# Optimization experiments

Measured on AMD Instinct MI355X. Metric: run time of the kernel, lower is better.

Reference implementation:

```python
import jax, jax.numpy as jnp
import numpy as np

B, N, MODEL_D = 2, 1024, 2048
KQ_D, V_D, H, I = 128, 128, 8, 4
ROPE_THETA = 10000.0


def _rope(x, theta):
    # x: [b, n, ..., d]; positions along axis 1, rotation over last dim d.
    d = x.shape[-1]
    n = x.shape[1]
    inv_freq = theta ** (-jnp.arange(0, d, 2, dtype=jnp.float32) / d)  # [d/2]
    ang = jnp.arange(n, dtype=jnp.float32)[:, None] * inv_freq          # [n, d/2]
    bshape = (1, n) + (1,) * (x.ndim - 3) + (d // 2,)
    cos = jnp.cos(ang).reshape(bshape).astype(x.dtype)
    sin = jnp.sin(ang).reshape(bshape).astype(x.dtype)
    x1, x2 = jnp.split(x, 2, axis=-1)
    return jnp.concatenate([x1 * cos - x2 * sin, x1 * sin + x2 * cos], axis=-1)


def setup_inputs() -> dict:
    key = jax.random.key(0)
    kx, kq, kk, kv, ko = jax.random.split(key, 5)
    s_in = 1.0 / np.sqrt(MODEL_D)
    s_out = 1.0 / np.sqrt(H * I * V_D)
    x = jax.random.normal(kx, (B, N, MODEL_D), jnp.float32)
    Wq = jax.random.normal(kq, (MODEL_D, H, I, KQ_D), jnp.float32) * s_in
    Wk = jax.random.normal(kk, (MODEL_D, H, KQ_D), jnp.float32) * s_in
    Wv = jax.random.normal(kv, (MODEL_D, H, V_D), jnp.float32) * s_in
    Wo = jax.random.normal(ko, (H, I, V_D, MODEL_D), jnp.float32) * s_out
    return {"x": x, "Wq": Wq, "Wk": Wk, "Wv": Wv, "Wo": Wo}


def reference(x, Wq, Wk, Wv, Wo):
    # GQA projections (per Ueajsum specs)
    q = jnp.einsum('bnd,dhik->bnhik', x, Wq)   # [B,N,H,I,K]
    k = jnp.einsum('bnd,dhc->bnhc', x, Wk)     # [B,N,H,K]
    v = jnp.einsum('bnd,dhv->bnhv', x, Wv)     # [B,N,H,V]
    # RoPE on q and k
    q = _rope(q, ROPE_THETA)
    k = _rope(k, ROPE_THETA)
    # Causal softmax attention, each kv head serves I query heads
    scale = 1.0 / np.sqrt(KQ_D)
    scores = jnp.einsum('bnhic,bmhc->bhinm', q, k) * scale  # [B,H,I,N,N]
    n = x.shape[1]
    causal = jnp.tril(jnp.ones((n, n), dtype=bool))
    scores = jnp.where(causal, scores, jnp.finfo(scores.dtype).min)
    p = jax.nn.softmax(scores, axis=-1)
    out = jnp.einsum('bhinm,bmhv->bnhiv', p, v)              # [B,N,H,I,V]
    return jnp.einsum('bnhiv,hivd->bnd', out, Wo)            # [B,N,D]
```

## Files before the change

kernel.cpp:

```cpp
#include <hip/hip_runtime.h>
#include <hip/hip_bf16.h>

typedef __bf16 bf16x8 __attribute__((ext_vector_type(8)));
typedef float floatx4 __attribute__((ext_vector_type(4)));

static __device__ __forceinline__ void async_cp16(const __bf16* g, __bf16* l) {
    typedef const __attribute__((address_space(1))) unsigned int gu32;
    typedef __attribute__((address_space(3))) unsigned int lu32;
    __builtin_amdgcn_global_load_lds((gu32*)g, (lu32*)l, 16, 0, 0);
}

static __device__ __forceinline__ void tile64_f32(
    const float* __restrict__ src, __bf16* __restrict__ dst,
    int R, int C, int r0, int c0, int tid, __bf16* t )
{
    {
        const int r = tid >> 2, cq = (tid & 3) * 16;
        const float* p = src + (size_t)(r0 + r) * C + c0 + cq;
        float4 f0 = *(const float4*)(p);
        float4 f1 = *(const float4*)(p + 4);
        float4 f2 = *(const float4*)(p + 8);
        float4 f3 = *(const float4*)(p + 12);
        __bf16 v[16] = {
            (__bf16)f0.x, (__bf16)f0.y, (__bf16)f0.z, (__bf16)f0.w,
            (__bf16)f1.x, (__bf16)f1.y, (__bf16)f1.z, (__bf16)f1.w,
            (__bf16)f2.x, (__bf16)f2.y, (__bf16)f2.z, (__bf16)f2.w,
            (__bf16)f3.x, (__bf16)f3.y, (__bf16)f3.z, (__bf16)f3.w };
        #pragma unroll
        for (int e = 0; e < 16; ++e) t[(cq + e) * 72 + r] = v[e];
    }
    __syncthreads();
    {
        const int c = tid >> 2, rq = (tid & 3) * 16;
        uint4 u0 = *(const uint4*)(&t[c * 72 + rq]);
        uint4 u1 = *(const uint4*)(&t[c * 72 + rq + 8]);
        __bf16* q = dst + (size_t)(c0 + c) * R + r0 + rq;
        *(uint4*)(q)     = u0;
        *(uint4*)(q + 8) = u1;
    }
}

static __device__ __forceinline__ void tile64_b16(
    const __bf16* __restrict__ src, __bf16* __restrict__ dst,
    int src_ld, int dst_ld, int tid, __bf16* t )
{
    {
        const int r = tid >> 2, cq = (tid & 3) * 16;
        const __bf16* p = src + (size_t)r * src_ld + cq;
        union { uint4 u; __bf16 b[8]; } a0, a1;
        a0.u = *(const uint4*)(p);
        a1.u = *(const uint4*)(p + 8);
        #pragma unroll
        for (int e = 0; e < 8; ++e) {
            t[(cq + e) * 72 + r]     = a0.b[e];
            t[(cq + 8 + e) * 72 + r] = a1.b[e];
        }
    }
    __syncthreads();
    {
        const int c = tid >> 2, rq = (tid & 3) * 16;
        uint4 u0 = *(const uint4*)(&t[c * 72 + rq]);
        uint4 u1 = *(const uint4*)(&t[c * 72 + rq + 8]);
        __bf16* q = dst + (size_t)c * dst_ld + rq;
        *(uint4*)(q)     = u0;
        *(uint4*)(q + 8) = u1;
    }
}

__global__ __launch_bounds__(256) void prep_kernel(
    const float* __restrict__ x,  __bf16* __restrict__ xb,
    const float* __restrict__ Wq, const float* __restrict__ Wk,
    const float* __restrict__ Wv, __bf16* __restrict__ Wt)
{
    __shared__ __bf16 t[64 * 72];
    const int bk  = blockIdx.x;
    const int tid = threadIdx.x;

    if (bk < 2048) {
        int ct = bk & 63, rt = bk >> 6;
        tile64_f32(Wq, Wt, 2048, 4096, rt * 64, ct * 64, tid, t);
    } else if (bk < 2560) {
        int idx = bk - 2048, ct = idx & 15, rt = idx >> 4;
        tile64_f32(Wk, Wt + (size_t)4096 * 2048, 2048, 1024, rt * 64, ct * 64, tid, t);
    } else if (bk < 3072) {
        int idx = bk - 2560, ct = idx & 15, rt = idx >> 4;
        tile64_f32(Wv, Wt + (size_t)5120 * 2048, 2048, 1024, rt * 64, ct * 64, tid, t);
    } else {
        int idx = (bk - 3072) * 256 + tid;
        const float* p = x + (size_t)idx * 8;
        float4 f0 = *(const float4*)p;
        float4 f1 = *(const float4*)(p + 4);
        union { uint4 u; __bf16 b[8]; } o;
        o.b[0] = (__bf16)f0.x; o.b[1] = (__bf16)f0.y; o.b[2] = (__bf16)f0.z; o.b[3] = (__bf16)f0.w;
        o.b[4] = (__bf16)f1.x; o.b[5] = (__bf16)f1.y; o.b[6] = (__bf16)f1.z; o.b[7] = (__bf16)f1.w;
        *(uint4*)(xb + (size_t)idx * 8) = o.u;
    }
}

__global__ __launch_bounds__(256) void rope_vtrans_wot_kernel(
    __bf16* __restrict__ qkv, __bf16* __restrict__ vt,
    const float* __restrict__ Wo, __bf16* __restrict__ WoT)
{
    __shared__ __bf16 t[64 * 72];
    const int bk  = blockIdx.x;
    const int tid = threadIdx.x;

    if (bk < 2560) {
        int idx  = bk * 256 + tid;
        int part = idx & 7;
        int tt   = idx >> 3;
        int head = tt % 40;
        int row  = tt / 40;
        int n    = row & 1023;
        int col0 = (head < 32) ? head * 128 : 4096 + (head - 32) * 128;
        size_t base = (size_t)row * 6144 + col0 + part * 8;

        union { uint4 u; __bf16 b[8]; } x1, x2, o1, o2;
        x1.u = *(const uint4*)(qkv + base);
        x2.u = *(const uint4*)(qkv + base + 64);
        #pragma unroll
        for (int e = 0; e < 8; ++e) {
            int j = part * 8 + e;
            float inv_freq = exp2f(-(float)j * 0.20762050593046015f);
            float ang = (float)n * inv_freq;
            float sv, cv;
            __sincosf(ang, &sv, &cv);
            float a = (float)x1.b[e], b2 = (float)x2.b[e];
            o1.b[e] = (__bf16)(a * cv - b2 * sv);
            o2.b[e] = (__bf16)(a * sv + b2 * cv);
        }
        *(uint4*)(qkv + base)      = o1.u;
        *(uint4*)(qkv + base + 64) = o2.u;
    } else if (bk < 3072) {
        int idx = bk - 2560;
        int bh = idx >> 5, rem = idx & 31;
        int k0 = (rem >> 1) * 64, v0 = (rem & 1) * 64;
        int b = bh >> 3, h = bh & 7;
        const __bf16* src = qkv + (size_t)(b * 1024 + k0) * 6144 + 5120 + h * 128 + v0;
        __bf16* dst = vt + ((size_t)bh * 128 + v0) * 1024 + k0;
        tile64_b16(src, dst, 6144, 1024, tid, t);
    } else {
        int idx = bk - 3072;
        int ct = idx & 31, rt = idx >> 5;
        tile64_f32(Wo, WoT, 4096, 2048, rt * 64, ct * 64, tid, t);
    }
}

__global__ __launch_bounds__(512) void gemm_bt(
    const __bf16* __restrict__ A,
    const __bf16* __restrict__ Bt,
    __bf16* __restrict__ C,
    int M, int lda, int ldb, int ldc,
    int kc_base, int kc_extra)
{
    __shared__ __bf16 As[2][256 * 64];
    __shared__ __bf16 Bs[2][256 * 64];

    const int tid  = threadIdx.x;
    const int wave = tid >> 6;
    const int lane = tid & 63;
    const int quad = lane >> 4;
    const int l15  = lane & 15;
    const int wr   = wave >> 2;
    const int wc   = wave & 3;

    const int bm = blockIdx.y * 256;
    const int bn = blockIdx.x * 256;
    const int z  = blockIdx.z;
    const int Kc = kc_base + ((z == (int)gridDim.z - 1) ? kc_extra : 0);
    const int NT = Kc >> 6;

    A  += (size_t)z * kc_base;
    Bt += (size_t)z * kc_base;
    C  += (size_t)z * M * ldc;

    floatx4 acc[32];
    #pragma unroll
    for (int i = 0; i < 32; ++i) acc[i] = floatx4{0.f, 0.f, 0.f, 0.f};

    const int sr = lane >> 3;
    const int sc = ((lane & 7) ^ sr) * 8;
    const __bf16* a0 = A  + (size_t)(bm + wave * 8 + sr) * lda + sc;
    const __bf16* b0 = Bt + (size_t)(bn + wave * 8 + sr) * ldb + sc;
    const int ldsw = wave * 512;

    const int arow = (wr * 128 + l15) * 64;
    const int brow = (wc * 64  + l15) * 64;
    const int cx0  = ((0 + quad) ^ (l15 & 7)) * 8;
    const int cx1  = ((4 + quad) ^ (l15 & 7)) * 8;

    #pragma unroll
    for (int q = 0; q < 4; ++q)
        async_cp16(a0 + (size_t)(q * 64) * lda, (__bf16*)&As[0][q * 4096 + ldsw]);
    #pragma unroll
    for (int q = 0; q < 4; ++q)
        async_cp16(b0 + (size_t)(q * 64) * ldb, (__bf16*)&Bs[0][q * 4096 + ldsw]);
    if (NT > 1) {
        #pragma unroll
        for (int q = 0; q < 4; ++q)
            async_cp16(a0 + (size_t)(q * 64) * lda + 64, (__bf16*)&As[1][q * 4096 + ldsw]);
        #pragma unroll
        for (int q = 0; q < 4; ++q)
            async_cp16(b0 + (size_t)(q * 64) * ldb + 64, (__bf16*)&Bs[1][q * 4096 + ldsw]);
        asm volatile("s_waitcnt vmcnt(8)" ::: "memory");
    } else {
        asm volatile("s_waitcnt vmcnt(0)" ::: "memory");
    }
    __builtin_amdgcn_s_barrier();
    __builtin_amdgcn_sched_barrier(0);

    for (int t = 0; t < NT; ++t) {
        const int cur = t & 1;
        const __bf16* Ac = As[cur];
        const __bf16* Bc = Bs[cur];
        __bf16* An = (__bf16*)As[cur];
        __bf16* Bn = (__bf16*)Bs[cur];

        bf16x8 af[4][2], bfA[2][2], bfB[2][2];

        #pragma unroll
        for (int tt = 0; tt < 4; ++tt) {
            af[tt][0] = *(const bf16x8*)(&Ac[arow + tt * 1024 + cx0]);
            af[tt][1] = *(const bf16x8*)(&Ac[arow + tt * 1024 + cx1]);
        }
        #pragma unroll
        for (int uu = 0; uu < 2; ++uu) {
            bfA[uu][0] = *(const bf16x8*)(&Bc[brow + uu * 1024 + cx0]);
            bfA[uu][1] = *(const bf16x8*)(&Bc[brow + uu * 1024 + cx1]);
        }
        __builtin_amdgcn_s_barrier();
        asm volatile("s_waitcnt lgkmcnt(0)" ::: "memory");
        __builtin_amdgcn_sched_barrier(0);
        __builtin_amdgcn_s_setprio(1);
        #pragma unroll
        for (int ko = 0; ko < 2; ++ko)
            #pragma unroll
            for (int tt = 0; tt < 4; ++tt)
                #pragma unroll
                for (int uu = 0; uu < 2; ++uu)
                    acc[tt * 4 + uu] = __builtin_amdgcn_mfma_f32_16x16x32_bf16(
                        af[tt][ko], bfA[uu][ko], acc[tt * 4 + uu], 0, 0, 0);
        __builtin_amdgcn_s_setprio(0);
        __builtin_amdgcn_s_barrier();
        __builtin_amdgcn_sched_barrier(0);

        #pragma unroll
        for (int uu = 0; uu < 2; ++uu) {
            bfB[uu][0] = *(const bf16x8*)(&Bc[brow + (2 + uu) * 1024 + cx0]);
            bfB[uu][1] = *(const bf16x8*)(&Bc[brow + (2 + uu) * 1024 + cx1]);
        }
        __builtin_amdgcn_s_barrier();
        asm volatile("s_waitcnt lgkmcnt(0)" ::: "memory");
        __builtin_amdgcn_sched_barrier(0);
        __builtin_amdgcn_s_setprio(1);
        #pragma unroll
        for (int ko = 0; ko < 2; ++ko)
            #pragma unroll
            for (int tt = 0; tt < 4; ++tt)
                #pragma unroll
                for (int uu = 0; uu < 2; ++uu)
                    acc[tt * 4 + 2 + uu] = __builtin_amdgcn_mfma_f32_16x16x32_bf16(
                        af[tt][ko], bfB[uu][ko], acc[tt * 4 + 2 + uu], 0, 0, 0);
        __builtin_amdgcn_s_setprio(0);
        __builtin_amdgcn_s_barrier();
        __builtin_amdgcn_sched_barrier(0);

        #pragma unroll
        for (int tt = 0; tt < 4; ++tt) {
            af[tt][0] = *(const bf16x8*)(&Ac[arow + (4 + tt) * 1024 + cx0]);
            af[tt][1] = *(const bf16x8*)(&Ac[arow + (4 + tt) * 1024 + cx1]);
        }
        if (t + 2 < NT) {
            #pragma unroll
            for (int q = 0; q < 4; ++q)
                async_cp16(b0 + (size_t)(q * 64) * ldb + (t + 2) * 64,
                           Bn + q * 4096 + ldsw);
        }
        __builtin_amdgcn_s_barrier();
        asm volatile("s_waitcnt lgkmcnt(0)" ::: "memory");
        __builtin_amdgcn_sched_barrier(0);
        __builtin_amdgcn_s_setprio(1);
        #pragma unroll
        for (int ko = 0; ko < 2; ++ko)
            #pragma unroll
            for (int tt = 0; tt < 4; ++tt)
                #pragma unroll
                for (int uu = 0; uu < 2; ++uu)
                    acc[(4 + tt) * 4 + uu] = __builtin_amdgcn_mfma_f32_16x16x32_bf16(
                        af[tt][ko], bfA[uu][ko], acc[(4 + tt) * 4 + uu], 0, 0, 0);
        __builtin_amdgcn_s_setprio(0);
        __builtin_amdgcn_s_barrier();
        __builtin_amdgcn_sched_barrier(0);

        if (t + 2 < NT) {
            #pragma unroll
            for (int q = 0; q < 4; ++q)
                async_cp16(a0 + (size_t)(q * 64) * lda + (t + 2) * 64,
                           An + q * 4096 + ldsw);
        }
        __builtin_amdgcn_s_setprio(1);
        #pragma unroll
        for (int ko = 0; ko < 2; ++ko)
            #pragma unroll
            for (int tt = 0; tt < 4; ++tt)
                #pragma unroll
                for (int uu = 0; uu < 2; ++uu)
                    acc[(4 + tt) * 4 + 2 + uu] = __builtin_amdgcn_mfma_f32_16x16x32_bf16(
                        af[tt][ko], bfB[uu][ko], acc[(4 + tt) * 4 + 2 + uu], 0, 0, 0);
        __builtin_amdgcn_s_setprio(0);
        if (t + 2 < NT) {
            asm volatile("s_waitcnt vmcnt(8)" ::: "memory");
        } else {
            asm volatile("s_waitcnt vmcnt(0)" ::: "memory");
        }
        __builtin_amdgcn_s_barrier();
        __builtin_amdgcn_sched_barrier(0);
    }

    #pragma unroll
    for (int tt = 0; tt < 8; ++tt)
        #pragma unroll
        for (int uu = 0; uu < 4; ++uu) {
            const int row = bm + wr * 128 + tt * 16 + quad * 4;
            const int col = bn + wc * 64 + uu * 16 + l15;
            #pragma unroll
            for (int r = 0; r < 4; ++r)
                C[(size_t)(row + r) * ldc + col] = (__bf16)acc[tt * 4 + uu][r];
        }
}

__global__ __launch_bounds__(256) void reduce_kernel(
    const __bf16* __restrict__ part, float* __restrict__ out)
{
    int idx = blockIdx.x * 256 + threadIdx.x;
    const size_t S = (size_t)2048 * 2048;
    union { uint4 u; __bf16 b[8]; } p0, p1, p2;
    p0.u = *(const uint4*)(part + (size_t)idx * 8);
    p1.u = *(const uint4*)(part + S + (size_t)idx * 8);
    p2.u = *(const uint4*)(part + 2 * S + (size_t)idx * 8);
    float4 o0, o1;
    o0.x = (float)p0.b[0] + (float)p1.b[0] + (float)p2.b[0];
    o0.y = (float)p0.b[1] + (float)p1.b[1] + (float)p2.b[1];
    o0.z = (float)p0.b[2] + (float)p1.b[2] + (float)p2.b[2];
    o0.w = (float)p0.b[3] + (float)p1.b[3] + (float)p2.b[3];
    o1.x = (float)p0.b[4] + (float)p1.b[4] + (float)p2.b[4];
    o1.y = (float)p0.b[5] + (float)p1.b[5] + (float)p2.b[5];
    o1.z = (float)p0.b[6] + (float)p1.b[6] + (float)p2.b[6];
    o1.w = (float)p0.b[7] + (float)p1.b[7] + (float)p2.b[7];
    *(float4*)(out + (size_t)idx * 8)     = o0;
    *(float4*)(out + (size_t)idx * 8 + 4) = o1;
}

__global__ __launch_bounds__(512, 2) void attn_kernel(
    const __bf16* __restrict__ qkv,
    const __bf16* __restrict__ vt,
    __bf16* __restrict__ ao)
{
    const int PS_LD = 72;
    __shared__ __bf16 Ks[64 * 128];
    __shared__ __bf16 Vs[128 * 64];
    __shared__ __bf16 Ps[8][16 * PS_LD];

    const int tid  = threadIdx.x;
    const int wave = tid >> 6;
    const int lane = tid & 63;
    const int quad = lane >> 4;
    const int l15  = lane & 15;
    const int i    = wave >> 1;
    const int rt   = wave & 1;

    const int pair = blockIdx.x;
    const int bh   = blockIdx.y;
    const int b    = bh >> 3, h = bh & 7;
    const __bf16* vtb = vt + (size_t)bh * 128 * 1024;

    const int keyA = wave * 8 + (lane >> 4);
    const int keyB = keyA + 4;
    const int chA  = (lane & 15) ^ (keyA & 15);
    const int chB  = (lane & 15) ^ (keyB & 15);
    const __bf16* gK0 = qkv + (size_t)(b * 1024 + keyA) * 6144 + 4096 + h * 128 + chA * 8;
    const __bf16* gK1 = qkv + (size_t)(b * 1024 + keyB) * 6144 + 4096 + h * 128 + chB * 8;
    __bf16* lK0 = Ks + (wave * 8) * 128;
    __bf16* lK1 = Ks + (wave * 8 + 4) * 128;

    const int vdA = wave * 16 + (lane >> 3);
    const int vdB = vdA + 8;
    const int cvA = (lane & 7) ^ (vdA & 7);
    const int cvB = (lane & 7) ^ (vdB & 7);
    const __bf16* gV0 = vtb + (size_t)vdA * 1024 + cvA * 8;
    const __bf16* gV1 = vtb + (size_t)vdB * 1024 + cvB * 8;
    __bf16* lV0 = Vs + (wave * 16) * 64;
    __bf16* lV1 = Vs + (wave * 16 + 8) * 64;

    bf16x8 onesf;
    #pragma unroll
    for (int j = 0; j < 8; ++j) onesf[j] = (__bf16)1.0f;

    const float C2 = 0.12751898549f;

    #pragma unroll
    for (int ph = 0; ph < 2; ++ph) {
        const int qt    = ph ? (31 - pair) : pair;
        const int qrow0 = qt * 32 + rt * 16;

        const __bf16* qp = qkv + (size_t)(b * 1024 + qrow0 + l15) * 6144 + (h * 4 + i) * 128;
        bf16x8 qf[4];
        #pragma unroll
        for (int c = 0; c < 4; ++c)
            qf[c] = *(const bf16x8*)(qp + c * 32 + quad * 8);

        floatx4 acc[8];
        #pragma unroll
        for (int u = 0; u < 8; ++u) acc[u] = floatx4{0.f, 0.f, 0.f, 0.f};
        floatx4 accl = floatx4{0.f, 0.f, 0.f, 0.f};

        const int ntiles = (qt >> 1) + 1;
        for (int t = 0; t < ntiles; ++t) {
            const int kt = t * 64;
            __syncthreads();
            async_cp16(gK0 + (size_t)kt * 6144, lK0);
            async_cp16(gK1 + (size_t)kt * 6144, lK1);
            async_cp16(gV0 + kt, lV0);
            async_cp16(gV1 + kt, lV1);
            __syncthreads();

            floatx4 s[4];
            #pragma unroll
            for (int ks = 0; ks < 4; ++ks) s[ks] = floatx4{0.f, 0.f, 0.f, 0.f};
            #pragma unroll
            for (int c = 0; c < 4; ++c) {
                #pragma unroll
                for (int ks = 0; ks < 4; ++ks) {
                    bf16x8 kf = *(const bf16x8*)(
                        &Ks[(ks * 16 + l15) * 128 + ((c * 4 + quad) ^ l15) * 8]);
                    s[ks] = __builtin_amdgcn_mfma_f32_16x16x32_bf16(qf[c], kf, s[ks], 0, 0, 0);
                }
            }

            #pragma unroll
            for (int r = 0; r < 4; ++r) {
                int qrow = qrow0 + quad * 4 + r;
                #pragma unroll
                for (int ks = 0; ks < 4; ++ks) {
                    int kc = kt + ks * 16 + l15;
                    float p = (kc <= qrow) ? exp2f(s[ks][r] * C2) : 0.0f;
                    Ps[wave][(quad * 4 + r) * PS_LD + ks * 16 + l15] = (__bf16)p;
                }
            }

            #pragma unroll
            for (int s2 = 0; s2 < 2; ++s2) {
                bf16x8 pa = *(const bf16x8*)(&Ps[wave][l15 * PS_LD + s2 * 32 + quad * 8]);
                accl = __builtin_amdgcn_mfma_f32_16x16x32_bf16(pa, onesf, accl, 0, 0, 0);
                #pragma unroll
                for (int u = 0; u < 8; ++u) {
                    bf16x8 vf = *(const bf16x8*)(
                        &Vs[(u * 16 + l15) * 64 + (((s2 * 4 + quad) ^ (l15 & 7))) * 8]);
                    acc[u] = __builtin_amdgcn_mfma_f32_16x16x32_bf16(pa, vf, acc[u], 0, 0, 0);
                }
            }
        }

        #pragma unroll
        for (int r = 0; r < 4; ++r) {
            float inv = 1.0f / accl[r];
            int row = qrow0 + quad * 4 + r;
            __bf16* op = ao + (size_t)(b * 1024 + row) * 4096 + (h * 4 + i) * 128;
            #pragma unroll
            for (int u = 0; u < 8; ++u)
                op[u * 16 + l15] = (__bf16)(acc[u][r] * inv);
        }
    }
}

extern "C" void kernel_launch(void* const* d_in, const int* in_sizes, int n_in,
                              void* d_out, int out_size, void* d_ws, size_t ws_size,
                              hipStream_t stream)
{
    const float* x  = (const float*)d_in[0];
    const float* Wq = (const float*)d_in[1];
    const float* Wk = (const float*)d_in[2];
    const float* Wv = (const float*)d_in[3];
    const float* Wo = (const float*)d_in[4];
    float* out = (float*)d_out;

    const size_t MB = 1024 * 1024;
    char* ws = (char*)d_ws;
    __bf16* qkv  = (__bf16*)(ws);
    __bf16* vtb  = (__bf16*)(ws + 24 * MB);
    __bf16* xb   = (__bf16*)(ws + 28 * MB);
    __bf16* Wt   = (__bf16*)(ws + 36 * MB);
    __bf16* WoT  = (__bf16*)(ws + 28 * MB);
    __bf16* ao   = (__bf16*)(ws + 44 * MB);
    __bf16* part = (__bf16*)(ws);

    prep_kernel<<<5120, 256, 0, stream>>>(x, xb, Wq, Wk, Wv, Wt);
    gemm_bt<<<dim3(24, 8), 512, 0, stream>>>(xb, Wt, qkv, 2048, 2048, 2048, 6144, 2048, 0);
    rope_vtrans_wot_kernel<<<5120, 256, 0, stream>>>(qkv, vtb, Wo, WoT);
    attn_kernel<<<dim3(16, 16), 512, 0, stream>>>(qkv, vtb, ao);
    gemm_bt<<<dim3(8, 8, 3), 512, 0, stream>>>(ao, WoT, part, 2048, 4096, 4096, 2048, 1344, 64);
    reduce_kernel<<<2048, 256, 0, stream>>>(part, out);
}
```

Baseline: 301.8 us.

## Software-pipeline GEMM main loop, deferring bottom-half MFMAs into next iteration

Restructures the bf16 MFMA GEMM main loop from four barrier-separated quadrant phases into a software-pipelined schedule. The bottom-half MFMAs (af1 x bf) are carried over and issued at the start of the next iteration, overlapping the LDS reads of the next tile's fragments, and a final epilogue handles the last ones. This cuts the workgroup barriers per K-step from several to about one and merges the async global-to-LDS copies for A and B into one spot. The cost is more live fragment registers across iterations, which could lower occupancy or cause spills, and a different ordering of LDS reads against the async copies.

```diff
diff --git a/kernel.cpp b/kernel.cpp
--- a/kernel.cpp
+++ b/kernel.cpp
@@ -209,6 +209,8 @@
     __builtin_amdgcn_s_barrier();
     __builtin_amdgcn_sched_barrier(0);
 
+    bf16x8 af1[4][2], bf[4][2];
+
     for (int t = 0; t < NT; ++t) {
         const int cur = t & 1;
         const __bf16* Ac = As[cur];
@@ -216,99 +218,68 @@
         __bf16* An = (__bf16*)As[cur];
         __bf16* Bn = (__bf16*)Bs[cur];
 
-        bf16x8 af[4][2], bfA[2][2], bfB[2][2];
-
+        bf16x8 af0[4][2];
         #pragma unroll
         for (int tt = 0; tt < 4; ++tt) {
-            af[tt][0] = *(const bf16x8*)(&Ac[arow + tt * 1024 + cx0]);
-            af[tt][1] = *(const bf16x8*)(&Ac[arow + tt * 1024 + cx1]);
-        }
-        #pragma unroll
-        for (int uu = 0; uu < 2; ++uu) {
-            bfA[uu][0] = *(const bf16x8*)(&Bc[brow + uu * 1024 + cx0]);
-            bfA[uu][1] = *(const bf16x8*)(&Bc[brow + uu * 1024 + cx1]);
-        }
-        __builtin_amdgcn_s_barrier();
+            af0[tt][0] = *(const bf16x8*)(&Ac[arow + tt * 1024 + cx0]);
+            af0[tt][1] = *(const bf16x8*)(&Ac[arow + tt * 1024 + cx1]);
+        }
+        __builtin_amdgcn_sched_barrier(0);
+
+        if (t) {
+            __builtin_amdgcn_s_setprio(1);
+            #pragma unroll
+            for (int ko = 0; ko < 2; ++ko)
+                #pragma unroll
+                for (int tt = 0; tt < 4; ++tt)
+                    #pragma unroll
+                    for (int uu = 0; uu < 4; ++uu)
+                        acc[(4 + tt) * 4 + uu] = __builtin_amdgcn_mfma_f32_16x16x32_bf16(
+                            af1[tt][ko], bf[uu][ko], acc[(4 + tt) * 4 + uu], 0, 0, 0);
+            __builtin_amdgcn_s_setprio(0);
+        }
+        __builtin_amdgcn_sched_barrier(0);
         asm volatile("s_waitcnt lgkmcnt(0)" ::: "memory");
         __builtin_amdgcn_sched_barrier(0);
+
+        #pragma unroll
+        for (int uu = 0; uu < 4; ++uu) {
+            bf[uu][0] = *(const bf16x8*)(&Bc[brow + uu * 1024 + cx0]);
+            bf[uu][1] = *(const bf16x8*)(&Bc[brow + uu * 1024 + cx1]);
+        }
+        #pragma unroll
+        for (int tt = 0; tt < 4; ++tt) {
+            af1[tt][0] = *(const bf16x8*)(&Ac[arow + (4 + tt) * 1024 + cx0]);
+            af1[tt][1] = *(const bf16x8*)(&Ac[arow + (4 + tt) * 1024 + cx1]);
+        }
+        __builtin_amdgcn_sched_barrier(0);
+        asm volatile("s_waitcnt lgkmcnt(8)" ::: "memory");
+        __builtin_amdgcn_sched_barrier(0);
+
         __builtin_amdgcn_s_setprio(1);
         #pragma unroll
         for (int ko = 0; ko < 2; ++ko)
             #pragma unroll
             for (int tt = 0; tt < 4; ++tt)
                 #pragma unroll
-                for (int uu = 0; uu < 2; ++uu)
+                for (int uu = 0; uu < 4; ++uu)
                     acc[tt * 4 + uu] = __builtin_amdgcn_mfma_f32_16x16x32_bf16(
-                        af[tt][ko], bfA[uu][ko], acc[tt * 4 + uu], 0, 0, 0);
+                        af0[tt][ko], bf[uu][ko], acc[tt * 4 + uu], 0, 0, 0);
         __builtin_amdgcn_s_setprio(0);
+        __builtin_amdgcn_sched_barrier(0);
+        asm volatile("s_waitcnt lgkmcnt(0)" ::: "memory");
+        __builtin_amdgcn_sched_barrier(0);
+
         __builtin_amdgcn_s_barrier();
-        __builtin_amdgcn_sched_barrier(0);
-
-        #pragma unroll
-        for (int uu = 0; uu < 2; ++uu) {
-            bfB[uu][0] = *(const bf16x8*)(&Bc[brow + (2 + uu) * 1024 + cx0]);
-            bfB[uu][1] = *(const bf16x8*)(&Bc[brow + (2 + uu) * 1024 + cx1]);
-        }
-        __builtin_amdgcn_s_barrier();
-        asm volatile("s_waitcnt lgkmcnt(0)" ::: "memory");
-        __builtin_amdgcn_sched_barrier(0);
-        __builtin_amdgcn_s_setprio(1);
-        #pragma unroll
-        for (int ko = 0; ko < 2; ++ko)
-            #pragma unroll
-            for (int tt = 0; tt < 4; ++tt)
-                #pragma unroll
-                for (int uu = 0; uu < 2; ++uu)
-                    acc[tt * 4 + 2 + uu] = __builtin_amdgcn_mfma_f32_16x16x32_bf16(
-                        af[tt][ko], bfB[uu][ko], acc[tt * 4 + 2 + uu], 0, 0, 0);
-        __builtin_amdgcn_s_setprio(0);
-        __builtin_amdgcn_s_barrier();
-        __builtin_amdgcn_sched_barrier(0);
-
-        #pragma unroll
-        for (int tt = 0; tt < 4; ++tt) {
-            af[tt][0] = *(const bf16x8*)(&Ac[arow + (4 + tt) * 1024 + cx0]);
-            af[tt][1] = *(const bf16x8*)(&Ac[arow + (4 + tt) * 1024 + cx1]);
-        }
         if (t + 2 < NT) {
+            #pragma unroll
+            for (int q = 0; q < 4; ++q)
+                async_cp16(a0 + (size_t)(q * 64) * lda + (t + 2) * 64,
+                           An + q * 4096 + ldsw);
             #pragma unroll
             for (int q = 0; q < 4; ++q)
                 async_cp16(b0 + (size_t)(q * 64) * ldb + (t + 2) * 64,
                            Bn + q * 4096 + ldsw);
-        }
-        __builtin_amdgcn_s_barrier();
-        asm volatile("s_waitcnt lgkmcnt(0)" ::: "memory");
-        __builtin_amdgcn_sched_barrier(0);
-        __builtin_amdgcn_s_setprio(1);
-        #pragma unroll
-        for (int ko = 0; ko < 2; ++ko)
-            #pragma unroll
-            for (int tt = 0; tt < 4; ++tt)
-                #pragma unroll
-                for (int uu = 0; uu < 2; ++uu)
-                    acc[(4 + tt) * 4 + uu] = __builtin_amdgcn_mfma_f32_16x16x32_bf16(
-                        af[tt][ko], bfA[uu][ko], acc[(4 + tt) * 4 + uu], 0, 0, 0);
-        __builtin_amdgcn_s_setprio(0);
-        __builtin_amdgcn_s_barrier();
-        __builtin_amdgcn_sched_barrier(0);
-
-        if (t + 2 < NT) {
-            #pragma unroll
-            for (int q = 0; q < 4; ++q)
-                async_cp16(a0 + (size_t)(q * 64) * lda + (t + 2) * 64,
-                           An + q * 4096 + ldsw);
-        }
-        __builtin_amdgcn_s_setprio(1);
-        #pragma unroll
-        for (int ko = 0; ko < 2; ++ko)
-            #pragma unroll
-            for (int tt = 0; tt < 4; ++tt)
-                #pragma unroll
-                for (int uu = 0; uu < 2; ++uu)
-                    acc[(4 + tt) * 4 + 2 + uu] = __builtin_amdgcn_mfma_f32_16x16x32_bf16(
-                        af[tt][ko], bfB[uu][ko], acc[(4 + tt) * 4 + 2 + uu], 0, 0, 0);
-        __builtin_amdgcn_s_setprio(0);
-        if (t + 2 < NT) {
             asm volatile("s_waitcnt vmcnt(8)" ::: "memory");
         } else {
             asm volatile("s_waitcnt vmcnt(0)" ::: "memory");
@@ -316,6 +287,17 @@
         __builtin_amdgcn_s_barrier();
         __builtin_amdgcn_sched_barrier(0);
     }
+
+    __builtin_amdgcn_s_setprio(1);
+    #pragma unroll
+    for (int ko = 0; ko < 2; ++ko)
+        #pragma unroll
+        for (int tt = 0; tt < 4; ++tt)
+            #pragma unroll
+            for (int uu = 0; uu < 4; ++uu)
+                acc[(4 + tt) * 4 + uu] = __builtin_amdgcn_mfma_f32_16x16x32_bf16(
+                    af1[tt][ko], bf[uu][ko], acc[(4 + tt) * 4 + uu], 0, 0, 0);
+    __builtin_amdgcn_s_setprio(0);
 
     #pragma unroll
     for (int tt = 0; tt < 8; ++tt)
```

After: 308.9 us. +2.4%, slower.
